# Optimization experiments

Measured on AMD Instinct MI355X. Metric: run time of the kernel, lower is better.

## Reference

```python
import jax, jax.numpy as jnp
import numpy as np

N_NODES = 100000

def gcn_conv(x, W, b, src, dst, n_nodes):
    # x: [N, Fin], W: [Fin, Fout], b: [Fout]; src/dst include self-loops.
    h = x @ W                                            # [N, Fout]
    deg = jnp.zeros((n_nodes,), x.dtype).at[dst].add(1.0)  # in-degree incl. self-loop
    dinv = jax.lax.rsqrt(deg)                            # deg >= 1 due to self-loops
    norm = dinv[src] * dinv[dst]                         # [E']
    msg = h[src] * norm[:, None]                         # [E', Fout]
    out = jax.ops.segment_sum(msg, dst, num_segments=n_nodes)
    return out + b

def setup_inputs() -> dict:
    key = jax.random.key(0)
    k1, k2, k3, k4, k5, k6 = jax.random.split(key, 6)
    in_c, hid_c, out_c = 128, 64, 32
    x = jax.random.normal(k1, (N_NODES, in_c), dtype=jnp.float32)
    edge_index = jax.random.randint(k2, (2, 1600000), 0, N_NODES, dtype=jnp.int64)
    # Glorot-ish init for weights
    W1 = jax.random.normal(k3, (in_c, hid_c), dtype=jnp.float32) / np.sqrt(in_c)
    b1 = jnp.zeros((hid_c,), dtype=jnp.float32)
    W2 = jax.random.normal(k4, (hid_c, out_c), dtype=jnp.float32) / np.sqrt(hid_c)
    b2 = jnp.zeros((out_c,), dtype=jnp.float32)
    return {"x": x, "edge_index": edge_index, "W1": W1, "b1": b1, "W2": W2, "b2": b2}

def reference(x, edge_index, W1, b1, W2, b2):
    n = x.shape[0]
    loops = jnp.arange(n, dtype=edge_index.dtype)
    src = jnp.concatenate([edge_index[0], loops])   # add self-loops
    dst = jnp.concatenate([edge_index[1], loops])
    h = gcn_conv(x, W1, b1, src, dst, n)
    h = jax.nn.relu(h)
    out = gcn_conv(h, W2, b2, src, dst, n)
    return out
```

## Files before the change

### kernel.cpp

```cpp
#include <hip/hip_runtime.h>
#include <hip/hip_bf16.h>


#define FIN1 128
#define FOUT1 64
#define FOUT2 32
#define PAD 64
#define NPB 200
#define NBUCKET 500
#define CAP 4096
#define EPB 4096

typedef unsigned int uint;
typedef unsigned short ushort;
typedef __attribute__((ext_vector_type(8))) short bf16x8;
typedef __attribute__((ext_vector_type(4))) float f32x4;

__device__ __forceinline__ ushort f2bf(float f) {
    uint u = __float_as_uint(f);
    return (ushort)((u + 0x7fffu + ((u >> 16) & 1u)) >> 16);
}
__device__ __forceinline__ float bf2f(ushort b) {
    return __uint_as_float(((uint)b) << 16);
}


__global__ __launch_bounds__(256) void bin_edges(const int* __restrict__ src,
                                                 const int* __restrict__ dst,
                                                 int* __restrict__ cursors,
                                                 int* __restrict__ binned, int e) {
    __shared__ int s_hist[NBUCKET];
    __shared__ int s_base[NBUCKET];
    __shared__ int s_cur[NBUCKET];
    const int t = threadIdx.x;
    for (int i = t; i < NBUCKET; i += 256) s_hist[i] = 0;
    __syncthreads();
    const int base = blockIdx.x * EPB;
    int vpk[16], vb[16];
#pragma unroll
    for (int k = 0; k < 16; ++k) {
        int idx = base + t + k * 256;
        bool ok = idx < e;
        int s = ok ? src[idx] : 0;
        int d = ok ? dst[idx] : 0;
        int bk = d / NPB;
        vb[k] = ok ? bk : -1;
        vpk[k] = s | ((d - bk * NPB) << 17);
        if (ok) atomicAdd(&s_hist[bk], 1);
    }
    __syncthreads();
    for (int i = t; i < NBUCKET; i += 256) {
        int h = s_hist[i];
        s_base[i] = (h > 0) ? atomicAdd(&cursors[i], h) : 0;
        s_cur[i] = 0;
    }
    __syncthreads();
#pragma unroll
    for (int k = 0; k < 16; ++k) {
        int bk = vb[k];
        if (bk >= 0) {
            int r = s_base[bk] + atomicAdd(&s_cur[bk], 1);
            if (r < CAP) binned[(size_t)bk * CAP + r] = vpk[k];
        }
    }
}


__global__ __launch_bounds__(256) void build_ell(const int* __restrict__ binned,
                                                 const int* __restrict__ cursors,
                                                 int* __restrict__ counts,
                                                 float* __restrict__ dinv,
                                                 int* __restrict__ ell, int n) {
    __shared__ int s_cnt[NPB];
    __shared__ int s_ell[NPB * PAD];
    const int b = blockIdx.x, t = threadIdx.x;
    for (int i = t; i < NPB; i += 256) s_cnt[i] = 0;
    __syncthreads();
    const int len = min(cursors[b], CAP);
    const int* edges = binned + (size_t)b * CAP;
    const int node0 = b * NPB;
    for (int i = t; i < len; i += 256) {
        int pk = edges[i];
        int local = pk >> 17;
        int r = atomicAdd(&s_cnt[local], 1);
        if (r < PAD) s_ell[local * PAD + r] = pk & 0x1FFFF;
    }
    __syncthreads();
    for (int i = t; i < NPB; i += 256) {
        int node = node0 + i;
        if (node < n) {
            int full = s_cnt[i];
            counts[node] = min(full, PAD);
            dinv[node] = rsqrtf((float)full + 1.0f);
        }
    }
    int4* d4 = (int4*)(ell + (size_t)node0 * PAD);
    const int4* s4 = (const int4*)s_ell;
    for (int i = t; i < NPB * PAD / 4; i += 256) d4[i] = s4[i];
}

template <int K, int F, int CT, int LOG2F>
__device__ __forceinline__ void stage_W(const float* __restrict__ W, ushort* sB, int t) {
    for (int sidx = t; sidx < K * F; sidx += 256) {
        int k = sidx >> LOG2F;
        int f = sidx & (F - 1);
        int kc = k >> 5, j = k & 7, quadb = (k >> 3) & 3;
        int c = f >> 4, nn = f & 15;
        int d = ((kc * CT + c) * 64 + quadb * 16 + nn) * 8 + j;
        sB[d] = f2bf(W[sidx]);
    }
}


template <int K, int F, int LOG2F>
__global__ __launch_bounds__(256) void gemm_mfma(const float* __restrict__ A,
                                                 const float* __restrict__ W,
                                                 const float* __restrict__ dinv,
                                                 ushort* __restrict__ out, int n) {
    constexpr int KC = K / 32;
    constexpr int CT = F / 16;
    __shared__ ushort sB[KC * CT * 64 * 8];
    const int t = threadIdx.x;
    stage_W<K, F, CT, LOG2F>(W, sB, t);
    __syncthreads();

    const int w = threadIdx.x >> 6;
    const int lane = threadIdx.x & 63;
    const int quad = lane >> 4;
    const int mcol = lane & 15;

    bf16x8 bfr[KC][CT];
    const bf16x8* sB8 = reinterpret_cast<const bf16x8*>(sB);
#pragma unroll
    for (int kc = 0; kc < KC; ++kc)
#pragma unroll
        for (int c = 0; c < CT; ++c)
            bfr[kc][c] = sB8[(kc * CT + c) * 64 + lane];

    const int ntiles = n / 16;
#pragma unroll
    for (int tt = 0; tt < 2; ++tt) {
        const int tile = (blockIdx.x * 4 + w) * 2 + tt;
        if (tile >= ntiles) continue;
        const int rb = tile * 16;
        bf16x8 afr[KC];
#pragma unroll
        for (int kc = 0; kc < KC; ++kc) {
            const float* ap = A + (size_t)(rb + mcol) * K + kc * 32 + quad * 8;
            float4 x0 = *reinterpret_cast<const float4*>(ap);
            float4 x1 = *reinterpret_cast<const float4*>(ap + 4);
            bf16x8 a;
            a[0] = (short)f2bf(x0.x); a[1] = (short)f2bf(x0.y);
            a[2] = (short)f2bf(x0.z); a[3] = (short)f2bf(x0.w);
            a[4] = (short)f2bf(x1.x); a[5] = (short)f2bf(x1.y);
            a[6] = (short)f2bf(x1.z); a[7] = (short)f2bf(x1.w);
            afr[kc] = a;
        }
        f32x4 acc[CT];
#pragma unroll
        for (int c = 0; c < CT; ++c) acc[c] = (f32x4){0.f, 0.f, 0.f, 0.f};
#pragma unroll
        for (int kc = 0; kc < KC; ++kc)
#pragma unroll
            for (int c = 0; c < CT; ++c)
                acc[c] = __builtin_amdgcn_mfma_f32_16x16x32_bf16(afr[kc], bfr[kc][c], acc[c], 0, 0, 0);
        float dv[4];
#pragma unroll
        for (int r = 0; r < 4; ++r) dv[r] = dinv[rb + quad * 4 + r];
#pragma unroll
        for (int c = 0; c < CT; ++c)
#pragma unroll
            for (int r = 0; r < 4; ++r)
                out[(size_t)(rb + quad * 4 + r) * F + c * 16 + mcol] = f2bf(acc[c][r] * dv[r]);
    }
}


#define SASTRIDE 72

__global__ __launch_bounds__(256) void agg_gemm2(const ushort* __restrict__ h,
                                                 const int* __restrict__ counts,
                                                 const int* __restrict__ ell,
                                                 const float* __restrict__ dinv,
                                                 const float* __restrict__ bias,
                                                 const float* __restrict__ W2,
                                                 ushort* __restrict__ out, int n) {
    constexpr int KC = 2;
    constexpr int CT = 2;
    __shared__ ushort sB[KC * CT * 64 * 8];
    __shared__ ushort sA[16 * SASTRIDE];
    const int t = threadIdx.x;
    stage_W<64, 32, CT, 5>(W2, sB, t);

    const int w = __builtin_amdgcn_readfirstlane(t >> 6);
    const int lane = t & 63;
    const int rb = blockIdx.x * 16;

    for (int i = 0; i < 4; ++i) {
        const int node = rb + w * 4 + i;
        const int cnt = counts[node];
        const int* __restrict__ row = ell + (size_t)node * PAD;
        float acc = bf2f(h[(size_t)node * 64 + lane]);
        int r = 0;
        for (; r + 16 <= cnt; r += 16) {
            float v[16];
#pragma unroll
            for (int u = 0; u < 16; ++u) v[u] = bf2f(h[(size_t)row[r + u] * 64 + lane]);
            float t0 = ((v[0] + v[1]) + (v[2] + v[3])) + ((v[4] + v[5]) + (v[6] + v[7]));
            float t1 = ((v[8] + v[9]) + (v[10] + v[11])) + ((v[12] + v[13]) + (v[14] + v[15]));
            acc += t0 + t1;
        }
        for (; r + 8 <= cnt; r += 8) {
            float v[8];
#pragma unroll
            for (int u = 0; u < 8; ++u) v[u] = bf2f(h[(size_t)row[r + u] * 64 + lane]);
            acc += ((v[0] + v[1]) + (v[2] + v[3])) + ((v[4] + v[5]) + (v[6] + v[7]));
        }
        for (; r + 4 <= cnt; r += 4) {
            float v[4];
#pragma unroll
            for (int u = 0; u < 4; ++u) v[u] = bf2f(h[(size_t)row[r + u] * 64 + lane]);
            acc += (v[0] + v[1]) + (v[2] + v[3]);
        }
        for (; r < cnt; ++r) acc += bf2f(h[(size_t)row[r] * 64 + lane]);
        float v = fmaxf(acc * dinv[node] + bias[lane], 0.0f);
        sA[(w * 4 + i) * SASTRIDE + lane] = f2bf(v);
    }
    __syncthreads();

    if (w < 2) {
        const int quad = lane >> 4;
        const int mcol = lane & 15;
        const bf16x8* sB8 = reinterpret_cast<const bf16x8*>(sB);
        f32x4 acc = (f32x4){0.f, 0.f, 0.f, 0.f};
#pragma unroll
        for (int kc = 0; kc < KC; ++kc) {
            bf16x8 afr = *reinterpret_cast<const bf16x8*>(&sA[mcol * SASTRIDE + kc * 32 + quad * 8]);
            bf16x8 bfr = sB8[(kc * CT + w) * 64 + lane];
            acc = __builtin_amdgcn_mfma_f32_16x16x32_bf16(afr, bfr, acc, 0, 0, 0);
        }
#pragma unroll
        for (int r = 0; r < 4; ++r) {
            int orow = rb + quad * 4 + r;
            out[(size_t)orow * 32 + w * 16 + mcol] = f2bf(acc[r] * dinv[orow]);
        }
    }
}


__global__ __launch_bounds__(256) void aggregate32_bf(const ushort* __restrict__ h,
                                                      const int* __restrict__ counts,
                                                      const int* __restrict__ ell,
                                                      const float* __restrict__ dinv,
                                                      const float* __restrict__ bias,
                                                      float* __restrict__ out, int n) {
    const int wv = __builtin_amdgcn_readfirstlane(threadIdx.x >> 6);
    const int node = blockIdx.x * 4 + wv;
    const int lane = threadIdx.x & 63;
    const int f = lane & 31;
    if (node >= n) return;
    const int cnt = counts[node];
    const int* __restrict__ row = ell + (size_t)node * PAD;
    float acc = bf2f(h[(size_t)node * 32 + f]);
    int r = 0;
    for (; r + 16 <= cnt; r += 16) {
        float v[16];
#pragma unroll
        for (int i = 0; i < 16; ++i) v[i] = bf2f(h[(size_t)row[r + i] * 32 + f]);
        float t0 = ((v[0] + v[1]) + (v[2] + v[3])) + ((v[4] + v[5]) + (v[6] + v[7]));
        float t1 = ((v[8] + v[9]) + (v[10] + v[11])) + ((v[12] + v[13]) + (v[14] + v[15]));
        acc += t0 + t1;
    }
    for (; r + 8 <= cnt; r += 8) {
        float v[8];
#pragma unroll
        for (int i = 0; i < 8; ++i) v[i] = bf2f(h[(size_t)row[r + i] * 32 + f]);
        acc += ((v[0] + v[1]) + (v[2] + v[3])) + ((v[4] + v[5]) + (v[6] + v[7]));
    }
    for (; r + 4 <= cnt; r += 4) {
        float v[4];
#pragma unroll
        for (int i = 0; i < 4; ++i) v[i] = bf2f(h[(size_t)row[r + i] * 32 + f]);
        acc += (v[0] + v[1]) + (v[2] + v[3]);
    }
    for (; r < cnt; ++r) acc += bf2f(h[(size_t)row[r] * 32 + f]);
    float v = acc * dinv[node] + bias[f];
    if (lane < 32) out[(size_t)node * 32 + f] = v;
}

extern "C" void kernel_launch(void* const* d_in, const int* in_sizes, int n_in,
                              void* d_out, int out_size, void* d_ws, size_t ws_size,
                              hipStream_t stream) {
    const float* x  = (const float*)d_in[0];
    const int*   ei = (const int*)d_in[1];
    const float* W1 = (const float*)d_in[2];
    const float* b1 = (const float*)d_in[3];
    const float* W2 = (const float*)d_in[4];
    const float* b2 = (const float*)d_in[5];
    float* out = (float*)d_out;

    const int N = in_sizes[0] / FIN1;
    const int E = in_sizes[1] / 2;
    const int* src = ei;
    const int* dst = ei + E;

    char* w = (char*)d_ws;
    size_t off = 0;
    auto alloc = [&](size_t bytes) -> char* {
        char* p = w + off;
        off = (off + bytes + 255) & ~(size_t)255;
        return p;
    };
    int*    cursors = (int*)alloc((size_t)NBUCKET * 4);
    int*    counts  = (int*)alloc((size_t)N * 4);
    float*  dinv    = (float*)alloc((size_t)N * 4);
    int*    binned  = (int*)alloc((size_t)NBUCKET * CAP * 4);
    int*    ell     = (int*)alloc((size_t)N * PAD * 4);
    ushort* hbf     = (ushort*)alloc((size_t)N * 64 * 2);
    ushort* h2bf    = (ushort*)alloc((size_t)N * 32 * 2);
    (void)ws_size;

    const int BINB = (E + EPB - 1) / EPB;
    const int GB = (N / 16 + 7) / 8;
    const int FB = N / 16;
    const int AB = (N + 3) / 4;

    hipMemsetAsync(cursors, 0, (size_t)NBUCKET * 4, stream);
    bin_edges<<<BINB, 256, 0, stream>>>(src, dst, cursors, binned, E);
    build_ell<<<NBUCKET, 256, 0, stream>>>(binned, cursors, counts, dinv, ell, N);

    gemm_mfma<FIN1, FOUT1, 6><<<GB, 256, 0, stream>>>(x, W1, dinv, hbf, N);
    agg_gemm2<<<FB, 256, 0, stream>>>(hbf, counts, ell, dinv, b1, W2, h2bf, N);
    aggregate32_bf<<<AB, 256, 0, stream>>>(h2bf, counts, ell, dinv, b2, out, N);
}
```

Measured before the change: 230.1 us.

## Split wavefront across neighbors with 8-byte vector gathers in aggregation kernels

```diff
diff --git a/kernel.cpp b/kernel.cpp
--- a/kernel.cpp
+++ b/kernel.cpp
@@ -14,6 +14,7 @@
 typedef unsigned int uint;
 typedef unsigned short ushort;
 typedef __attribute__((ext_vector_type(8))) short bf16x8;
+typedef __attribute__((ext_vector_type(4))) short bf16x4;
 typedef __attribute__((ext_vector_type(4))) float f32x4;
 
 __device__ __forceinline__ ushort f2bf(float f) {
@@ -195,36 +196,54 @@
     const int w = __builtin_amdgcn_readfirstlane(t >> 6);
     const int lane = t & 63;
     const int rb = blockIdx.x * 16;
+    const int sub = lane >> 4;
+    const int fq = lane & 15;
 
     for (int i = 0; i < 4; ++i) {
         const int node = rb + w * 4 + i;
         const int cnt = counts[node];
         const int* __restrict__ row = ell + (size_t)node * PAD;
-        float acc = bf2f(h[(size_t)node * 64 + lane]);
+        f32x4 acc = (f32x4){0.f, 0.f, 0.f, 0.f};
+        if (sub == 0) {
+            bf16x4 sv = *reinterpret_cast<const bf16x4*>(h + (size_t)node * 64 + fq * 4);
+#pragma unroll
+            for (int j = 0; j < 4; ++j) acc[j] += bf2f((ushort)sv[j]);
+        }
         int r = 0;
         for (; r + 16 <= cnt; r += 16) {
-            float v[16];
-#pragma unroll
-            for (int u = 0; u < 16; ++u) v[u] = bf2f(h[(size_t)row[r + u] * 64 + lane]);
-            float t0 = ((v[0] + v[1]) + (v[2] + v[3])) + ((v[4] + v[5]) + (v[6] + v[7]));
-            float t1 = ((v[8] + v[9]) + (v[10] + v[11])) + ((v[12] + v[13]) + (v[14] + v[15]));
-            acc += t0 + t1;
-        }
-        for (; r + 8 <= cnt; r += 8) {
-            float v[8];
-#pragma unroll
-            for (int u = 0; u < 8; ++u) v[u] = bf2f(h[(size_t)row[r + u] * 64 + lane]);
-            acc += ((v[0] + v[1]) + (v[2] + v[3])) + ((v[4] + v[5]) + (v[6] + v[7]));
-        }
-        for (; r + 4 <= cnt; r += 4) {
-            float v[4];
-#pragma unroll
-            for (int u = 0; u < 4; ++u) v[u] = bf2f(h[(size_t)row[r + u] * 64 + lane]);
-            acc += (v[0] + v[1]) + (v[2] + v[3]);
-        }
-        for (; r < cnt; ++r) acc += bf2f(h[(size_t)row[r] * 64 + lane]);
-        float v = fmaxf(acc * dinv[node] + bias[lane], 0.0f);
-        sA[(w * 4 + i) * SASTRIDE + lane] = f2bf(v);
+            int4 iv = *reinterpret_cast<const int4*>(row + r + 4 * sub);
+            bf16x4 g0 = *reinterpret_cast<const bf16x4*>(h + (size_t)iv.x * 64 + fq * 4);
+            bf16x4 g1 = *reinterpret_cast<const bf16x4*>(h + (size_t)iv.y * 64 + fq * 4);
+            bf16x4 g2 = *reinterpret_cast<const bf16x4*>(h + (size_t)iv.z * 64 + fq * 4);
+            bf16x4 g3 = *reinterpret_cast<const bf16x4*>(h + (size_t)iv.w * 64 + fq * 4);
+#pragma unroll
+            for (int j = 0; j < 4; ++j)
+                acc[j] += (bf2f((ushort)g0[j]) + bf2f((ushort)g1[j])) +
+                          (bf2f((ushort)g2[j]) + bf2f((ushort)g3[j]));
+        }
+        for (; r < cnt; r += 4) {
+            if (sub < cnt - r) {
+                int idx = row[r + sub];
+                bf16x4 g = *reinterpret_cast<const bf16x4*>(h + (size_t)idx * 64 + fq * 4);
+#pragma unroll
+                for (int j = 0; j < 4; ++j) acc[j] += bf2f((ushort)g[j]);
+            }
+        }
+#pragma unroll
+        for (int j = 0; j < 4; ++j) {
+            acc[j] += __shfl_xor(acc[j], 16, 64);
+            acc[j] += __shfl_xor(acc[j], 32, 64);
+        }
+        if (sub == 0) {
+            const float dv = dinv[node];
+            const float4 bv = *reinterpret_cast<const float4*>(bias + fq * 4);
+            bf16x4 o;
+            o[0] = (short)f2bf(fmaxf(acc[0] * dv + bv.x, 0.0f));
+            o[1] = (short)f2bf(fmaxf(acc[1] * dv + bv.y, 0.0f));
+            o[2] = (short)f2bf(fmaxf(acc[2] * dv + bv.z, 0.0f));
+            o[3] = (short)f2bf(fmaxf(acc[3] * dv + bv.w, 0.0f));
+            *reinterpret_cast<bf16x4*>(&sA[(w * 4 + i) * SASTRIDE + fq * 4]) = o;
+        }
     }
     __syncthreads();
 
@@ -257,35 +276,50 @@
     const int wv = __builtin_amdgcn_readfirstlane(threadIdx.x >> 6);
     const int node = blockIdx.x * 4 + wv;
     const int lane = threadIdx.x & 63;
-    const int f = lane & 31;
+    const int sub = lane >> 3;
+    const int fq = lane & 7;
     if (node >= n) return;
     const int cnt = counts[node];
     const int* __restrict__ row = ell + (size_t)node * PAD;
-    float acc = bf2f(h[(size_t)node * 32 + f]);
+    f32x4 acc = (f32x4){0.f, 0.f, 0.f, 0.f};
+    if (sub == 0) {
+        bf16x4 sv = *reinterpret_cast<const bf16x4*>(h + (size_t)node * 32 + fq * 4);
+#pragma unroll
+        for (int j = 0; j < 4; ++j) acc[j] += bf2f((ushort)sv[j]);
+    }
     int r = 0;
     for (; r + 16 <= cnt; r += 16) {
-        float v[16];
-#pragma unroll
-        for (int i = 0; i < 16; ++i) v[i] = bf2f(h[(size_t)row[r + i] * 32 + f]);
-        float t0 = ((v[0] + v[1]) + (v[2] + v[3])) + ((v[4] + v[5]) + (v[6] + v[7]));
-        float t1 = ((v[8] + v[9]) + (v[10] + v[11])) + ((v[12] + v[13]) + (v[14] + v[15]));
-        acc += t0 + t1;
-    }
-    for (; r + 8 <= cnt; r += 8) {
-        float v[8];
-#pragma unroll
-        for (int i = 0; i < 8; ++i) v[i] = bf2f(h[(size_t)row[r + i] * 32 + f]);
-        acc += ((v[0] + v[1]) + (v[2] + v[3])) + ((v[4] + v[5]) + (v[6] + v[7]));
-    }
-    for (; r + 4 <= cnt; r += 4) {
-        float v[4];
-#pragma unroll
-        for (int i = 0; i < 4; ++i) v[i] = bf2f(h[(size_t)row[r + i] * 32 + f]);
-        acc += (v[0] + v[1]) + (v[2] + v[3]);
-    }
-    for (; r < cnt; ++r) acc += bf2f(h[(size_t)row[r] * 32 + f]);
-    float v = acc * dinv[node] + bias[f];
-    if (lane < 32) out[(size_t)node * 32 + f] = v;
+        int2 iv = *reinterpret_cast<const int2*>(row + r + 2 * sub);
+        bf16x4 g0 = *reinterpret_cast<const bf16x4*>(h + (size_t)iv.x * 32 + fq * 4);
+        bf16x4 g1 = *reinterpret_cast<const bf16x4*>(h + (size_t)iv.y * 32 + fq * 4);
+#pragma unroll
+        for (int j = 0; j < 4; ++j)
+            acc[j] += bf2f((ushort)g0[j]) + bf2f((ushort)g1[j]);
+    }
+    for (; r < cnt; r += 8) {
+        if (sub < cnt - r) {
+            int idx = row[r + sub];
+            bf16x4 g = *reinterpret_cast<const bf16x4*>(h + (size_t)idx * 32 + fq * 4);
+#pragma unroll
+            for (int j = 0; j < 4; ++j) acc[j] += bf2f((ushort)g[j]);
+        }
+    }
+#pragma unroll
+    for (int j = 0; j < 4; ++j) {
+        acc[j] += __shfl_xor(acc[j], 8, 64);
+        acc[j] += __shfl_xor(acc[j], 16, 64);
+        acc[j] += __shfl_xor(acc[j], 32, 64);
+    }
+    if (sub == 0) {
+        const float dv = dinv[node];
+        const float4 bv = *reinterpret_cast<const float4*>(bias + fq * 4);
+        float4 o;
+        o.x = acc[0] * dv + bv.x;
+        o.y = acc[1] * dv + bv.y;
+        o.z = acc[2] * dv + bv.z;
+        o.w = acc[3] * dv + bv.w;
+        *reinterpret_cast<float4*>(out + (size_t)node * 32 + fq * 4) = o;
+    }
 }
 
 extern "C" void kernel_launch(void* const* d_in, const int* in_sizes, int n_in,
```

Result: slower. 237.2 us (+3.1%).

## Pad ELL rows to multiples of eight and interleave four nodes per wave in aggregation

Applied to the files above, without the earlier changes.

```diff
diff --git a/kernel.cpp b/kernel.cpp
--- a/kernel.cpp
+++ b/kernel.cpp
@@ -75,6 +75,11 @@
     __shared__ int s_ell[NPB * PAD];
     const int b = blockIdx.x, t = threadIdx.x;
     for (int i = t; i < NPB; i += 256) s_cnt[i] = 0;
+    {
+        int4 pv = make_int4(n, n, n, n);
+        int4* s4 = (int4*)s_ell;
+        for (int i = t; i < NPB * PAD / 4; i += 256) s4[i] = pv;
+    }
     __syncthreads();
     const int len = min(cursors[b], CAP);
     const int* edges = binned + (size_t)b * CAP;
@@ -90,7 +95,7 @@
         int node = node0 + i;
         if (node < n) {
             int full = s_cnt[i];
-            counts[node] = min(full, PAD);
+            counts[node] = min((full + 7) & ~7, PAD);
             dinv[node] = rsqrtf((float)full + 1.0f);
         }
     }
@@ -195,36 +200,39 @@
     const int w = __builtin_amdgcn_readfirstlane(t >> 6);
     const int lane = t & 63;
     const int rb = blockIdx.x * 16;
-
+    const int node0 = rb + w * 4;
+
+    int cnt[4];
+    const int* rows[4];
+    float acc[4];
+#pragma unroll
     for (int i = 0; i < 4; ++i) {
-        const int node = rb + w * 4 + i;
-        const int cnt = counts[node];
-        const int* __restrict__ row = ell + (size_t)node * PAD;
-        float acc = bf2f(h[(size_t)node * 64 + lane]);
-        int r = 0;
-        for (; r + 16 <= cnt; r += 16) {
-            float v[16];
-#pragma unroll
-            for (int u = 0; u < 16; ++u) v[u] = bf2f(h[(size_t)row[r + u] * 64 + lane]);
-            float t0 = ((v[0] + v[1]) + (v[2] + v[3])) + ((v[4] + v[5]) + (v[6] + v[7]));
-            float t1 = ((v[8] + v[9]) + (v[10] + v[11])) + ((v[12] + v[13]) + (v[14] + v[15]));
-            acc += t0 + t1;
-        }
-        for (; r + 8 <= cnt; r += 8) {
-            float v[8];
-#pragma unroll
-            for (int u = 0; u < 8; ++u) v[u] = bf2f(h[(size_t)row[r + u] * 64 + lane]);
-            acc += ((v[0] + v[1]) + (v[2] + v[3])) + ((v[4] + v[5]) + (v[6] + v[7]));
-        }
-        for (; r + 4 <= cnt; r += 4) {
-            float v[4];
-#pragma unroll
-            for (int u = 0; u < 4; ++u) v[u] = bf2f(h[(size_t)row[r + u] * 64 + lane]);
-            acc += (v[0] + v[1]) + (v[2] + v[3]);
-        }
-        for (; r < cnt; ++r) acc += bf2f(h[(size_t)row[r] * 64 + lane]);
-        float v = fmaxf(acc * dinv[node] + bias[lane], 0.0f);
-        sA[(w * 4 + i) * SASTRIDE + lane] = f2bf(v);
+        cnt[i] = counts[node0 + i];
+        rows[i] = ell + (size_t)(node0 + i) * PAD;
+        acc[i] = bf2f(h[(size_t)(node0 + i) * 64 + lane]);
+    }
+    const int cmax = max(max(cnt[0], cnt[1]), max(cnt[2], cnt[3]));
+    for (int r = 0; r < cmax; r += 8) {
+        float v[4][8];
+#pragma unroll
+        for (int i = 0; i < 4; ++i) {
+            if (r < cnt[i]) {
+#pragma unroll
+                for (int u = 0; u < 8; ++u)
+                    v[i][u] = bf2f(h[(size_t)rows[i][r + u] * 64 + lane]);
+            }
+        }
+#pragma unroll
+        for (int i = 0; i < 4; ++i) {
+            if (r < cnt[i])
+                acc[i] += ((v[i][0] + v[i][1]) + (v[i][2] + v[i][3])) +
+                          ((v[i][4] + v[i][5]) + (v[i][6] + v[i][7]));
+        }
+    }
+#pragma unroll
+    for (int i = 0; i < 4; ++i) {
+        float vv = fmaxf(acc[i] * dinv[node0 + i] + bias[lane], 0.0f);
+        sA[(w * 4 + i) * SASTRIDE + lane] = f2bf(vv);
     }
     __syncthreads();
 
@@ -232,17 +240,17 @@
         const int quad = lane >> 4;
         const int mcol = lane & 15;
         const bf16x8* sB8 = reinterpret_cast<const bf16x8*>(sB);
-        f32x4 acc = (f32x4){0.f, 0.f, 0.f, 0.f};
+        f32x4 acc2 = (f32x4){0.f, 0.f, 0.f, 0.f};
 #pragma unroll
         for (int kc = 0; kc < KC; ++kc) {
             bf16x8 afr = *reinterpret_cast<const bf16x8*>(&sA[mcol * SASTRIDE + kc * 32 + quad * 8]);
             bf16x8 bfr = sB8[(kc * CT + w) * 64 + lane];
-            acc = __builtin_amdgcn_mfma_f32_16x16x32_bf16(afr, bfr, acc, 0, 0, 0);
+            acc2 = __builtin_amdgcn_mfma_f32_16x16x32_bf16(afr, bfr, acc2, 0, 0, 0);
         }
 #pragma unroll
         for (int r = 0; r < 4; ++r) {
             int orow = rb + quad * 4 + r;
-            out[(size_t)orow * 32 + w * 16 + mcol] = f2bf(acc[r] * dinv[orow]);
+            out[(size_t)orow * 32 + w * 16 + mcol] = f2bf(acc2[r] * dinv[orow]);
         }
     }
 }
@@ -255,37 +263,42 @@
                                                       const float* __restrict__ bias,
                                                       float* __restrict__ out, int n) {
     const int wv = __builtin_amdgcn_readfirstlane(threadIdx.x >> 6);
-    const int node = blockIdx.x * 4 + wv;
     const int lane = threadIdx.x & 63;
     const int f = lane & 31;
-    if (node >= n) return;
-    const int cnt = counts[node];
-    const int* __restrict__ row = ell + (size_t)node * PAD;
-    float acc = bf2f(h[(size_t)node * 32 + f]);
-    int r = 0;
-    for (; r + 16 <= cnt; r += 16) {
-        float v[16];
-#pragma unroll
-        for (int i = 0; i < 16; ++i) v[i] = bf2f(h[(size_t)row[r + i] * 32 + f]);
-        float t0 = ((v[0] + v[1]) + (v[2] + v[3])) + ((v[4] + v[5]) + (v[6] + v[7]));
-        float t1 = ((v[8] + v[9]) + (v[10] + v[11])) + ((v[12] + v[13]) + (v[14] + v[15]));
-        acc += t0 + t1;
-    }
-    for (; r + 8 <= cnt; r += 8) {
-        float v[8];
-#pragma unroll
-        for (int i = 0; i < 8; ++i) v[i] = bf2f(h[(size_t)row[r + i] * 32 + f]);
-        acc += ((v[0] + v[1]) + (v[2] + v[3])) + ((v[4] + v[5]) + (v[6] + v[7]));
-    }
-    for (; r + 4 <= cnt; r += 4) {
-        float v[4];
-#pragma unroll
-        for (int i = 0; i < 4; ++i) v[i] = bf2f(h[(size_t)row[r + i] * 32 + f]);
-        acc += (v[0] + v[1]) + (v[2] + v[3]);
-    }
-    for (; r < cnt; ++r) acc += bf2f(h[(size_t)row[r] * 32 + f]);
-    float v = acc * dinv[node] + bias[f];
-    if (lane < 32) out[(size_t)node * 32 + f] = v;
+    const int node0 = blockIdx.x * 16 + wv * 4;
+
+    int cnt[4];
+    const int* rows[4];
+    float acc[4];
+#pragma unroll
+    for (int i = 0; i < 4; ++i) {
+        cnt[i] = counts[node0 + i];
+        rows[i] = ell + (size_t)(node0 + i) * PAD;
+        acc[i] = bf2f(h[(size_t)(node0 + i) * 32 + f]);
+    }
+    const int cmax = max(max(cnt[0], cnt[1]), max(cnt[2], cnt[3]));
+    for (int r = 0; r < cmax; r += 8) {
+        float v[4][8];
+#pragma unroll
+        for (int i = 0; i < 4; ++i) {
+            if (r < cnt[i]) {
+#pragma unroll
+                for (int u = 0; u < 8; ++u)
+                    v[i][u] = bf2f(h[(size_t)rows[i][r + u] * 32 + f]);
+            }
+        }
+#pragma unroll
+        for (int i = 0; i < 4; ++i) {
+            if (r < cnt[i])
+                acc[i] += ((v[i][0] + v[i][1]) + (v[i][2] + v[i][3])) +
+                          ((v[i][4] + v[i][5]) + (v[i][6] + v[i][7]));
+        }
+    }
+    if (lane < 32) {
+#pragma unroll
+        for (int i = 0; i < 4; ++i)
+            out[(size_t)(node0 + i) * 32 + f] = acc[i] * dinv[node0 + i] + bias[f];
+    }
 }
 
 extern "C" void kernel_launch(void* const* d_in, const int* in_sizes, int n_in,
@@ -316,16 +329,18 @@
     float*  dinv    = (float*)alloc((size_t)N * 4);
     int*    binned  = (int*)alloc((size_t)NBUCKET * CAP * 4);
     int*    ell     = (int*)alloc((size_t)N * PAD * 4);
-    ushort* hbf     = (ushort*)alloc((size_t)N * 64 * 2);
-    ushort* h2bf    = (ushort*)alloc((size_t)N * 32 * 2);
+    ushort* hbf     = (ushort*)alloc((size_t)(N + 1) * 64 * 2);
+    ushort* h2bf    = (ushort*)alloc((size_t)(N + 1) * 32 * 2);
     (void)ws_size;
 
     const int BINB = (E + EPB - 1) / EPB;
     const int GB = (N / 16 + 7) / 8;
     const int FB = N / 16;
-    const int AB = (N + 3) / 4;
+    const int AB = N / 16;
 
     hipMemsetAsync(cursors, 0, (size_t)NBUCKET * 4, stream);
+    hipMemsetAsync(hbf + (size_t)N * 64, 0, 64 * 2, stream);
+    hipMemsetAsync(h2bf + (size_t)N * 32, 0, 32 * 2, stream);
     bin_edges<<<BINB, 256, 0, stream>>>(src, dst, cursors, binned, E);
     build_ell<<<NBUCKET, 256, 0, stream>>>(binned, cursors, counts, dinv, ell, N);
 
```

After: 228.7 us. No clear change (-0.6%).
